# Performance work log

Hardware: AMD Instinct MI355X
Metric: run time of the kernel (lower is better)

The kernel has to match this reference:

```python
import jax, jax.numpy as jnp
import numpy as np

N, NFEAT, NHID, NCLASS, E = 100000, 128, 128, 40, 1600000

def _glorot(key, fan_in, fan_out):
    lim = float(np.sqrt(6.0 / (fan_in + fan_out)))
    return jax.random.uniform(key, (fan_in, fan_out), jnp.float32, -lim, lim)

def setup_inputs() -> dict:
    key = jax.random.key(0)
    ks = jax.random.split(key, 20)
    inp = {
        'x': jax.random.normal(ks[0], (N, NFEAT), jnp.float32),
        'edge_index': jax.random.randint(ks[1], (2, E), 0, N, jnp.int64 if jax.config.x64_enabled else jnp.int32),
    }
    dims = [(NFEAT, NHID), (NHID, NHID), (NHID, NHID), (NHID, NHID), (NHID, NHID), (NHID, NHID)]
    names = ['gc1_w1', 'gc1_w2', 'gc2_w1', 'gc2_w2', 'gc3_w1', 'gc3_w2']
    for i, (nm, (fi, fo)) in enumerate(zip(names, dims)):
        inp[nm] = _glorot(ks[2 + i], fi, fo)
        inp[nm.replace('w', 'b')] = jnp.zeros((fo,), jnp.float32)
    inp['lin1_w'] = _glorot(ks[10], 3 * NHID, 3 * NHID)
    inp['lin1_b'] = jnp.zeros((3 * NHID,), jnp.float32)
    inp['lin2_w'] = _glorot(ks[11], 3 * NHID, NCLASS)
    inp['lin2_b'] = jnp.zeros((NCLASS,), jnp.float32)
    return inp

def _gin_conv(x, src, dst, w1, b1, w2, b2):
    # GINConv, eps=0: mlp(x + sum_{j->i} x_j)
    agg = jax.ops.segment_sum(x[src], dst, num_segments=N)  # [N, d]
    h = jax.nn.relu((x + agg) @ w1 + b1)
    return jax.nn.relu(h @ w2 + b2)

def reference(x, edge_index, gc1_w1, gc1_b1, gc1_w2, gc1_b2,
              gc2_w1, gc2_b1, gc2_w2, gc2_b2,
              gc3_w1, gc3_b1, gc3_w2, gc3_b2,
              lin1_w, lin1_b, lin2_w, lin2_b):
    src, dst = edge_index[0], edge_index[1]
    h1 = _gin_conv(x, src, dst, gc1_w1, gc1_b1, gc1_w2, gc1_b2)
    h2 = _gin_conv(h1, src, dst, gc2_w1, gc2_b1, gc2_w2, gc2_b2)
    h3 = _gin_conv(h2, src, dst, gc3_w1, gc3_b1, gc3_w2, gc3_b2)
    h = jnp.concatenate([h1, h2, h3], axis=1)  # [N, 3*nhid]
    h = jax.nn.relu(h @ lin1_w + lin1_b)  # dropout inactive in eval mode
    h = h @ lin2_w + lin2_b
    return jax.nn.log_softmax(h, axis=1)
```

## Files before the change

kernel.cpp:

```cpp
#include <hip/hip_runtime.h>

#define N_NODES 100000
#define NEDGE   1600000
#define NHID    128
#define NCLASS  40

#define AGG_NODES 128
#define COLV_LDS  3072
#define FILL_RANGE  12500
#define WPREP_TOT   264192
#define EPB 2048
#define NBB 782
#define SUBN 782
#define NSUB 16

using bf16x8 = __attribute__((ext_vector_type(8))) short;
using f32x4  = __attribute__((ext_vector_type(4))) float;

__device__ __forceinline__ float bf2f(unsigned short s) {
    unsigned u = ((unsigned)s) << 16; float f; __builtin_memcpy(&f, &u, 4); return f;
}
__device__ __forceinline__ unsigned short f2bf(float f) {
    unsigned u; __builtin_memcpy(&u, &f, 4);
    u = u + 0x7fffu + ((u >> 16) & 1u);
    return (unsigned short)(u >> 16);
}

__device__ __forceinline__ void gld16(const void* g, void* l) {
    __builtin_amdgcn_global_load_lds(g, l, 16, 0, 0);
}

__global__ __launch_bounds__(256) void k_bucket(const int* __restrict__ ei,
                                                unsigned* __restrict__ pairs,
                                                int* __restrict__ bofs, int* __restrict__ bcnt) {
    __shared__ int wcnt[4][8];
    __shared__ int wbase[4][8];
    __shared__ int sbase[9];
    const int tid = threadIdx.x, lane = tid & 63, w = tid >> 6;
    const int e0 = blockIdx.x * EPB;
    const unsigned long long below = (1ull << lane) - 1ull;

    int dl[8], src[8], sl[8], posw[8];
    int cnt[8] = {0, 0, 0, 0, 0, 0, 0, 0};
    #pragma unroll
    for (int k = 0; k < 8; ++k) {
        int e = e0 + w * 512 + k * 64 + lane;
        bool v = e < NEDGE;
        int d = v ? ei[NEDGE + e] : -1;
        src[k] = v ? ei[e] : 0;
        int slc = v ? d / FILL_RANGE : -1;
        sl[k] = slc;
        dl[k] = v ? d - slc * FILL_RANGE : 0;
        posw[k] = 0;
        #pragma unroll
        for (int s = 0; s < 8; ++s) {
            unsigned long long mask = __ballot(slc == s);
            if (slc == s) posw[k] = cnt[s] + (int)__popcll(mask & below);
            cnt[s] += (int)__popcll(mask);
        }
    }
    if (lane == 0) {
        #pragma unroll
        for (int s = 0; s < 8; ++s) wcnt[w][s] = cnt[s];
    }
    __syncthreads();
    if (tid == 0) {
        int run = 0;
        for (int s = 0; s < 8; ++s) {
            sbase[s] = run;
            for (int w2 = 0; w2 < 4; ++w2) { wbase[w2][s] = run; run += wcnt[w2][s]; }
        }
        sbase[8] = run;
        for (int s = 0; s < 8; ++s) {
            bofs[blockIdx.x * 8 + s] = e0 + sbase[s];
            bcnt[blockIdx.x * 8 + s] = sbase[s + 1] - sbase[s];
        }
    }
    __syncthreads();
    #pragma unroll
    for (int k = 0; k < 8; ++k) {
        if (sl[k] >= 0)
            pairs[e0 + wbase[w][sl[k]] + posw[k]] = ((unsigned)dl[k] << 17) | (unsigned)src[k];
    }
}

__global__ void k_sseg(const int* __restrict__ bcnt, int* __restrict__ pbase, int* __restrict__ stot) {
    __shared__ int sh[256];
    const int s = blockIdx.x, t = threadIdx.x;
    int v[4]; int sum = 0;
    #pragma unroll
    for (int k = 0; k < 4; ++k) {
        int i = t * 4 + k;
        v[k] = (i < NBB) ? bcnt[i * 8 + s] : 0;
        sum += v[k];
    }
    sh[t] = sum; __syncthreads();
    for (int off = 1; off < 256; off <<= 1) {
        int x = (t >= off) ? sh[t - off] : 0;
        __syncthreads();
        sh[t] += x;
        __syncthreads();
    }
    int excl = sh[t] - sum;
    #pragma unroll
    for (int k = 0; k < 4; ++k) {
        int i = t * 4 + k;
        if (i < NBB) pbase[i * 8 + s] = excl;
        excl += v[k];
    }
    if (t == 255) stot[s] = sh[255];
}

__global__ void k_sbase(const int* __restrict__ stot, int* __restrict__ sbase,
                        unsigned* __restrict__ pairs2) {
    if (threadIdx.x || blockIdx.x) return;
    int run = 0;
    for (int s = 0; s < 8; ++s) {
        sbase[s] = run;
        int end = run + stot[s];
        run = (end + 3) & ~3;
        for (int i = end; i < run; ++i) pairs2[i] = 0xFFFFFFFFu;
    }
    sbase[8] = run;
}

__global__ __launch_bounds__(256) void k_scatter(const unsigned* __restrict__ pairs,
                                                 const int* __restrict__ bcnt,
                                                 const int* __restrict__ pbase,
                                                 const int* __restrict__ sbase,
                                                 unsigned* __restrict__ pairs2) {
    __shared__ int lb[9], ldst[8];
    const int bb = blockIdx.x, tid = threadIdx.x;
    if (tid == 0) {
        int run = 0;
        for (int s = 0; s < 8; ++s) {
            lb[s] = run; run += bcnt[bb * 8 + s];
            ldst[s] = sbase[s] + pbase[bb * 8 + s];
        }
        lb[8] = run;
    }
    __syncthreads();
    const int nblk = lb[8];
    for (int i = tid; i < nblk; i += 256) {
        int s = 0;
        #pragma unroll
        for (int j = 1; j < 8; ++j) s += (i >= lb[j]);
        pairs2[ldst[s] + (i - lb[s])] = pairs[(size_t)bb * EPB + i];
    }
}

__global__ __launch_bounds__(512) void k_cnt4(const unsigned* __restrict__ pairs2,
                                              const int* __restrict__ sbase,
                                              int* __restrict__ cnt) {
    __shared__ int lcnt[SUBN];
    const int s = blockIdx.x & 7, sub = blockIdx.x >> 3;
    const int nlo = sub * SUBN;
    const int nhi = (nlo + SUBN < FILL_RANGE) ? nlo + SUBN : FILL_RANGE;
    const int tid = threadIdx.x;
    for (int i = tid; i < SUBN; i += 512) lcnt[i] = 0;
    __syncthreads();
    const int beg = sbase[s];
    const int n4 = (sbase[s + 1] - beg) >> 2;
    const uint4* p4 = (const uint4*)(pairs2 + beg);
    for (int i = tid; i < n4; i += 512) {
        uint4 q = p4[i];
        int d0 = (int)(q.x >> 17), d1 = (int)(q.y >> 17);
        int d2 = (int)(q.z >> 17), d3 = (int)(q.w >> 17);
        if (d0 >= nlo && d0 < nhi) atomicAdd(&lcnt[d0 - nlo], 1);
        if (d1 >= nlo && d1 < nhi) atomicAdd(&lcnt[d1 - nlo], 1);
        if (d2 >= nlo && d2 < nhi) atomicAdd(&lcnt[d2 - nlo], 1);
        if (d3 >= nlo && d3 < nhi) atomicAdd(&lcnt[d3 - nlo], 1);
    }
    __syncthreads();
    const int base = s * FILL_RANGE + nlo;
    for (int i = tid; i < nhi - nlo; i += 512) cnt[base + i] = lcnt[i];
}

__global__ void k_scan1(const int* __restrict__ cnt, int* __restrict__ rp, int* __restrict__ bsum) {
    __shared__ int sh[256];
    int t = threadIdx.x, base = blockIdx.x * 1024;
    int v[4]; int s = 0;
    for (int k = 0; k < 4; ++k) { int i = base + t * 4 + k; v[k] = (i < N_NODES) ? cnt[i] : 0; s += v[k]; }
    sh[t] = s; __syncthreads();
    for (int off = 1; off < 256; off <<= 1) {
        int x = (t >= off) ? sh[t - off] : 0;
        __syncthreads();
        sh[t] += x;
        __syncthreads();
    }
    int excl = sh[t] - s;
    for (int k = 0; k < 4; ++k) { int i = base + t * 4 + k; if (i < N_NODES) rp[i] = excl; excl += v[k]; }
    if (t == 255) bsum[blockIdx.x] = sh[255];
}

__global__ void k_scan2(int* __restrict__ bsum, int nb) {
    __shared__ int sh[256];
    int t = threadIdx.x;
    int v = (t < nb) ? bsum[t] : 0;
    sh[t] = v; __syncthreads();
    for (int off = 1; off < 256; off <<= 1) {
        int x = (t >= off) ? sh[t - off] : 0;
        __syncthreads();
        sh[t] += x;
        __syncthreads();
    }
    if (t < nb) bsum[t] = sh[t] - v;
}

__global__ void k_scan3(int* __restrict__ rp, const int* __restrict__ bsum) {
    int base = blockIdx.x * 1024;
    int off = bsum[blockIdx.x];
    for (int k = 0; k < 4; ++k) {
        int i = base + threadIdx.x * 4 + k;
        if (i < N_NODES) rp[i] += off;
    }
    if (blockIdx.x == 0 && threadIdx.x == 0) rp[N_NODES] = NEDGE;
}

__global__ __launch_bounds__(512) void k_fill4(const unsigned* __restrict__ pairs2,
                                               const int* __restrict__ sbase,
                                               const int* __restrict__ rp,
                                               int* __restrict__ colv) {
    __shared__ int lcur[SUBN];
    __shared__ int lrp[SUBN];
    const int s = blockIdx.x & 7, sub = blockIdx.x >> 3;
    const int nlo = sub * SUBN;
    const int nhi = (nlo + SUBN < FILL_RANGE) ? nlo + SUBN : FILL_RANGE;
    const int tid = threadIdx.x;
    const int gbase = s * FILL_RANGE + nlo;
    for (int i = tid; i < SUBN; i += 512) {
        lcur[i] = 0;
        lrp[i] = (i < nhi - nlo) ? rp[gbase + i] : 0;
    }
    __syncthreads();
    const int beg = sbase[s];
    const int n4 = (sbase[s + 1] - beg) >> 2;
    const uint4* p4 = (const uint4*)(pairs2 + beg);
    for (int i = tid; i < n4; i += 512) {
        uint4 q = p4[i];
        unsigned e[4] = {q.x, q.y, q.z, q.w};
        #pragma unroll
        for (int k = 0; k < 4; ++k) {
            int dl = (int)(e[k] >> 17);
            if (dl >= nlo && dl < nhi) {
                int li = dl - nlo;
                int pos = atomicAdd(&lcur[li], 1);
                colv[lrp[li] + pos] = (int)(e[k] & 0x1FFFFu);
            }
        }
    }
}

__global__ void k_wprep_all(const float* __restrict__ g0, const float* __restrict__ g1,
                            const float* __restrict__ g2, const float* __restrict__ g3,
                            const float* __restrict__ g4, const float* __restrict__ g5,
                            const float* __restrict__ l1w, const float* __restrict__ l2w,
                            unsigned short* __restrict__ dst) {
    int idx = blockIdx.x * 256 + threadIdx.x;
    if (idx >= WPREP_TOT) return;
    const float* w; int local, K, O;
    if (idx < 98304) {
        int r = idx >> 14; local = idx & 16383; K = 128; O = 128;
        w = r == 0 ? g0 : r == 1 ? g1 : r == 2 ? g2 : r == 3 ? g3 : r == 4 ? g4 : g5;
    } else if (idx < 245760) {
        local = idx - 98304; K = 384; O = 384; w = l1w;
    } else {
        local = idx - 245760; K = 384; O = 40; w = l2w;
    }
    int kss = K >> 5;
    int e = local & 7, lane = (local >> 3) & 63, rest = local >> 9;
    int ks = rest % kss, ot = rest / kss;
    int c = ot * 16 + (lane & 15);
    int k = ks * 32 + (lane >> 4) * 8 + e;
    float v = (c < O) ? w[k * O + c] : 0.f;
    dst[idx] = f2bf(v);
}

__global__ void k_xprep(const float* __restrict__ x, unsigned short* __restrict__ xs) {
    int s = blockIdx.x & 3;
    int rest = (blockIdx.x >> 2) * 256 + threadIdx.x;
    if (rest >= N_NODES * 16) return;
    int n = rest >> 4, wrd = rest & 15;
    float2 v = *(const float2*)(x + (size_t)n * 128 + s * 32 + wrd * 2);
    ((unsigned*)xs)[(size_t)s * N_NODES * 16 + rest] =
        (unsigned)f2bf(v.x) | ((unsigned)f2bf(v.y) << 16);
}

__device__ __forceinline__ void acc8(float* acc, uint4 f, float m) {
    unsigned u[4] = {f.x, f.y, f.z, f.w};
    for (int d = 0; d < 4; ++d) {
        acc[2 * d]     = fmaf(m, bf2f((unsigned short)u[d]), acc[2 * d]);
        acc[2 * d + 1] = fmaf(m, bf2f((unsigned short)(u[d] >> 16)), acc[2 * d + 1]);
    }
}

__global__ __launch_bounds__(512) void k_aggs(const unsigned short* __restrict__ feat,
                                              unsigned short* __restrict__ tout,
                                              const int* __restrict__ rp,
                                              const int* __restrict__ colv) {
    __shared__ int scol[COLV_LDS + 8];
    __shared__ int srp[AGG_NODES + 1];
    const int s = blockIdx.x & 3;
    const int chunk = blockIdx.x >> 2;
    const int tid = threadIdx.x;
    const int nbase = chunk * AGG_NODES;

    for (int i = tid; i <= AGG_NODES; i += 512) {
        int n = nbase + i;
        srp[i] = rp[n <= N_NODES ? n : N_NODES];
    }
    __syncthreads();
    const int ebase = srp[0];
    const int ecount = srp[AGG_NODES] - ebase;
    const int elds = ecount < COLV_LDS ? ecount : COLV_LDS;
    for (int i = tid; i < elds; i += 512) scol[i] = colv[ebase + i];
    if (tid < 8) scol[elds + tid] = 0;
    __syncthreads();

    const unsigned* fs = (const unsigned*)feat + (size_t)s * N_NODES * 16;
    unsigned* ts = (unsigned*)tout + (size_t)s * N_NODES * 16;

    const int sub = tid >> 2, q = tid & 3;
    const int node = nbase + sub;
    if (node >= N_NODES) return;
    const int off = q * 4;
    const int e0 = srp[sub] - ebase, e1 = srp[sub + 1] - ebase;

    float acc[8];
    {
        uint4 a = *(const uint4*)(fs + (size_t)node * 16 + off);
        unsigned u[4] = {a.x, a.y, a.z, a.w};
        for (int d = 0; d < 4; ++d) {
            acc[2 * d]     = bf2f((unsigned short)u[d]);
            acc[2 * d + 1] = bf2f((unsigned short)(u[d] >> 16));
        }
    }

    if (ecount <= COLV_LDS) {
        int e = e0;
        const int efull = e0 + ((e1 - e0) & ~7);
        for (; e < efull; e += 8) {
            int j[8];
            #pragma unroll
            for (int k = 0; k < 8; ++k) j[k] = scol[e + k];
            uint4 f[8];
            #pragma unroll
            for (int k = 0; k < 8; ++k)
                f[k] = *(const uint4*)(fs + (size_t)j[k] * 16 + off);
            #pragma unroll
            for (int k = 0; k < 8; ++k) acc8(acc, f[k], 1.f);
        }
        if (e < e1) {
            int j[8]; float m[8];
            #pragma unroll
            for (int k = 0; k < 8; ++k) {
                int ee = e + k;
                bool v = ee < e1;
                j[k] = v ? scol[ee] : node;
                m[k] = v ? 1.f : 0.f;
            }
            uint4 f[8];
            #pragma unroll
            for (int k = 0; k < 8; ++k)
                f[k] = *(const uint4*)(fs + (size_t)j[k] * 16 + off);
            #pragma unroll
            for (int k = 0; k < 8; ++k) acc8(acc, f[k], m[k]);
        }
    } else {
        for (int e = e0; e < e1; e += 8) {
            int j[8]; float m[8];
            #pragma unroll
            for (int k = 0; k < 8; ++k) {
                int ee = e + k;
                bool v = ee < e1;
                int idx = ee < COLV_LDS ? scol[ee] : colv[ebase + ee];
                j[k] = v ? idx : node;
                m[k] = v ? 1.f : 0.f;
            }
            uint4 f[8];
            #pragma unroll
            for (int k = 0; k < 8; ++k)
                f[k] = *(const uint4*)(fs + (size_t)j[k] * 16 + off);
            #pragma unroll
            for (int k = 0; k < 8; ++k) acc8(acc, f[k], m[k]);
        }
    }

    uint4 o;
    o.x = (unsigned)f2bf(acc[0]) | ((unsigned)f2bf(acc[1]) << 16);
    o.y = (unsigned)f2bf(acc[2]) | ((unsigned)f2bf(acc[3]) << 16);
    o.z = (unsigned)f2bf(acc[4]) | ((unsigned)f2bf(acc[5]) << 16);
    o.w = (unsigned)f2bf(acc[6]) | ((unsigned)f2bf(acc[7]) << 16);
    *(uint4*)(ts + (size_t)node * 16 + off) = o;
}

__global__ __launch_bounds__(512) void k_mlp(
    const unsigned short* __restrict__ tin,
    const unsigned short* __restrict__ w1t, const float* __restrict__ b1,
    const unsigned short* __restrict__ w2t, const float* __restrict__ b2,
    unsigned short* __restrict__ hout) {
    __shared__ __align__(16) char tlds[4 * 8192];
    __shared__ __align__(16) char hlds[4 * 8192];
    const int tid = threadIdx.x, lane = tid & 63, w = tid >> 6;
    const int l15 = lane & 15, lg = lane >> 4;
    const int nbase = blockIdx.x * 128;
    const int rx = (l15 >> 1) & 3;

    #pragma unroll
    for (int i = 0; i < 4; ++i) {
        int c = w + i * 8;
        int s = c >> 3, rblk = c & 7;
        int node = nbase + rblk * 16 + (lane >> 2);
        if (node >= N_NODES) node = 0;
        int hsrc = (lane & 3) ^ ((lane >> 3) & 3);
        gld16(tin + ((size_t)s * N_NODES + node) * 32 + hsrc * 8,
              tlds + c * 1024);
    }

    bf16x8 B1[4], B2[4];
    const int col = w * 16 + l15;
    const float bias1 = b1[col], bias2 = b2[col];
    #pragma unroll
    for (int ks = 0; ks < 4; ++ks) {
        B1[ks] = *(const bf16x8*)(w1t + ((size_t)(w * 4 + ks) * 64 + lane) * 8);
        B2[ks] = *(const bf16x8*)(w2t + ((size_t)(w * 4 + ks) * 64 + lane) * 8);
    }
    __syncthreads();

    {
        const int hoff = ((lg ^ rx) << 4);
        bf16x8 A[2][4];
        #pragma unroll
        for (int ks = 0; ks < 4; ++ks)
            A[0][ks] = *(const bf16x8*)(tlds + ks * 8192 + l15 * 64 + hoff);
        #pragma unroll
        for (int m = 0; m < 8; ++m) {
            int cur = m & 1, nxt = cur ^ 1;
            if (m < 7) {
                int row = (m + 1) * 16 + l15;
                #pragma unroll
                for (int ks = 0; ks < 4; ++ks)
                    A[nxt][ks] = *(const bf16x8*)(tlds + ks * 8192 + row * 64 + hoff);
            }
            f32x4 acc = {0.f, 0.f, 0.f, 0.f};
            #pragma unroll
            for (int ks = 0; ks < 4; ++ks)
                acc = __builtin_amdgcn_mfma_f32_16x16x32_bf16(A[cur][ks], B1[ks], acc, 0, 0, 0);
            #pragma unroll
            for (int r = 0; r < 4; ++r) {
                int row = m * 16 + lg * 4 + r;
                int rw = (2 * lg + (r >> 1)) & 3;
                int h = (w & 1) * 2 + (l15 >> 3);
                float v = acc[r] + bias1; v = v > 0.f ? v : 0.f;
                *(unsigned short*)(hlds + (w >> 1) * 8192 + row * 64 +
                                   ((h ^ rw) << 4) + (l15 & 7) * 2) = f2bf(v);
            }
        }
    }
    __syncthreads();

    {
        const int hoff = ((lg ^ rx) << 4);
        bf16x8 A[2][4];
        #pragma unroll
        for (int ks = 0; ks < 4; ++ks)
            A[0][ks] = *(const bf16x8*)(hlds + ks * 8192 + l15 * 64 + hoff);
        #pragma unroll
        for (int m = 0; m < 8; ++m) {
            int cur = m & 1, nxt = cur ^ 1;
            if (m < 7) {
                int row = (m + 1) * 16 + l15;
                #pragma unroll
                for (int ks = 0; ks < 4; ++ks)
                    A[nxt][ks] = *(const bf16x8*)(hlds + ks * 8192 + row * 64 + hoff);
            }
            f32x4 acc = {0.f, 0.f, 0.f, 0.f};
            #pragma unroll
            for (int ks = 0; ks < 4; ++ks)
                acc = __builtin_amdgcn_mfma_f32_16x16x32_bf16(A[cur][ks], B2[ks], acc, 0, 0, 0);
            #pragma unroll
            for (int r = 0; r < 4; ++r) {
                int node = nbase + m * 16 + lg * 4 + r;
                if (node < N_NODES) {
                    float v = acc[r] + bias2; v = v > 0.f ? v : 0.f;
                    hout[((size_t)(w >> 1) * N_NODES + node) * 32 + (w & 1) * 16 + l15] = f2bf(v);
                }
            }
        }
    }
}

__global__ __launch_bounds__(512, 4) void k_final(
    const unsigned short* __restrict__ h1, const unsigned short* __restrict__ h2,
    const unsigned short* __restrict__ h3,
    const unsigned short* __restrict__ l1t, const float* __restrict__ l1b,
    const unsigned short* __restrict__ l2t, const float* __restrict__ l2b,
    float* __restrict__ out) {
    __shared__ __align__(16) char lds[12 * 4096];
    const int tid = threadIdx.x, lane = tid & 63, w = tid >> 6;
    const int l15 = lane & 15, lg = lane >> 4;
    const int nbase = blockIdx.x * 64;
    const int rx = (l15 >> 1) & 3;

    #pragma unroll
    for (int i = 0; i < 6; ++i) {
        int c = w + i * 8;
        int g = c >> 2, rblk = c & 3;
        int part = g >> 2, slice = g & 3;
        int node = nbase + rblk * 16 + (lane >> 2);
        if (node >= N_NODES) node = 0;
        int hsrc = (lane & 3) ^ ((lane >> 3) & 3);
        const unsigned short* hp = part == 0 ? h1 : (part == 1 ? h2 : h3);
        gld16(hp + ((size_t)slice * N_NODES + node) * 32 + hsrc * 8,
              lds + c * 1024);
    }

    bf16x8 B[2][3];
    #pragma unroll
    for (int ot = 0; ot < 3; ++ot)
        B[0][ot] = *(const bf16x8*)(l1t + ((size_t)((w * 3 + ot) * 12) * 64 + lane) * 8);
    __syncthreads();

    f32x4 acc[4][3];
    #pragma unroll
    for (int m = 0; m < 4; ++m)
        #pragma unroll
        for (int ot = 0; ot < 3; ++ot) acc[m][ot] = {0.f, 0.f, 0.f, 0.f};
    {
        const int hoff = ((lg ^ rx) << 4);
        #pragma unroll
        for (int ks = 0; ks < 12; ++ks) {
            int cur = ks & 1, nxt = cur ^ 1;
            if (ks < 11) {
                #pragma unroll
                for (int ot = 0; ot < 3; ++ot)
                    B[nxt][ot] = *(const bf16x8*)(l1t + ((size_t)((w * 3 + ot) * 12 + ks + 1) * 64 + lane) * 8);
            }
            bf16x8 A[4];
            #pragma unroll
            for (int m = 0; m < 4; ++m) {
                int row = m * 16 + l15;
                A[m] = *(const bf16x8*)(lds + ks * 4096 + row * 64 + hoff);
            }
            #pragma unroll
            for (int ot = 0; ot < 3; ++ot)
                #pragma unroll
                for (int m = 0; m < 4; ++m)
                    acc[m][ot] = __builtin_amdgcn_mfma_f32_16x16x32_bf16(A[m], B[cur][ot], acc[m][ot], 0, 0, 0);
        }
    }
    __syncthreads();

    #pragma unroll
    for (int ot = 0; ot < 3; ++ot) {
        int c = (w * 3 + ot) * 16 + l15;
        int gc = c >> 5, h = (c >> 3) & 3, b2i = (c & 7) * 2;
        float bias = l1b[c];
        #pragma unroll
        for (int m = 0; m < 4; ++m)
            #pragma unroll
            for (int r = 0; r < 4; ++r) {
                int row = m * 16 + lg * 4 + r;
                int rw = (2 * lg + (r >> 1)) & 3;
                float v = acc[m][ot][r] + bias; v = v > 0.f ? v : 0.f;
                *(unsigned short*)(lds + gc * 4096 + row * 64 + ((h ^ rw) << 4) + b2i) = f2bf(v);
            }
    }
    __syncthreads();

    if (w < 4) {
        f32x4 acc2[3];
        #pragma unroll
        for (int ot = 0; ot < 3; ++ot) acc2[ot] = {0.f, 0.f, 0.f, 0.f};
        {
            const int row = w * 16 + l15;
            const int hoff = ((lg ^ rx) << 4);
            bf16x8 C2[2][3];
            #pragma unroll
            for (int ot = 0; ot < 3; ++ot)
                C2[0][ot] = *(const bf16x8*)(l2t + ((size_t)(ot * 12) * 64 + lane) * 8);
            #pragma unroll
            for (int ks = 0; ks < 12; ++ks) {
                int cur = ks & 1, nxt = cur ^ 1;
                if (ks < 11) {
                    #pragma unroll
                    for (int ot = 0; ot < 3; ++ot)
                        C2[nxt][ot] = *(const bf16x8*)(l2t + ((size_t)(ot * 12 + ks + 1) * 64 + lane) * 8);
                }
                bf16x8 A2 = *(const bf16x8*)(lds + ks * 4096 + row * 64 + hoff);
                #pragma unroll
                for (int ot = 0; ot < 3; ++ot)
                    acc2[ot] = __builtin_amdgcn_mfma_f32_16x16x32_bf16(A2, C2[cur][ot], acc2[ot], 0, 0, 0);
            }
        }

        int c0 = l15;
        #pragma unroll
        for (int r = 0; r < 4; ++r) {
            float v0 = acc2[0][r] + l2b[c0];
            float v1 = acc2[1][r] + l2b[c0 + 16];
            float v2 = (c0 < 8) ? (acc2[2][r] + l2b[c0 + 32]) : -1e30f;
            float mx = fmaxf(fmaxf(v0, v1), v2);
            for (int msk = 1; msk < 16; msk <<= 1) mx = fmaxf(mx, __shfl_xor(mx, msk));
            float s = __expf(v0 - mx) + __expf(v1 - mx) + ((c0 < 8) ? __expf(v2 - mx) : 0.f);
            for (int msk = 1; msk < 16; msk <<= 1) s += __shfl_xor(s, msk);
            float lse = mx + __logf(s);
            int node = nbase + w * 16 + lg * 4 + r;
            if (node < N_NODES) {
                out[(size_t)node * 40 + c0] = v0 - lse;
                out[(size_t)node * 40 + c0 + 16] = v1 - lse;
                if (c0 < 8) out[(size_t)node * 40 + c0 + 32] = v2 - lse;
            }
        }
    }
}

extern "C" void kernel_launch(void* const* d_in, const int* in_sizes, int n_in,
                              void* d_out, int out_size, void* d_ws, size_t ws_size,
                              hipStream_t stream) {
    const float* x  = (const float*)d_in[0];
    const int*   ei = (const int*)d_in[1];
    const float* gw1[3] = {(const float*)d_in[2],  (const float*)d_in[6],  (const float*)d_in[10]};
    const float* gb1[3] = {(const float*)d_in[3],  (const float*)d_in[7],  (const float*)d_in[11]};
    const float* gw2[3] = {(const float*)d_in[4],  (const float*)d_in[8],  (const float*)d_in[12]};
    const float* gb2[3] = {(const float*)d_in[5],  (const float*)d_in[9],  (const float*)d_in[13]};
    const float* l1w = (const float*)d_in[14];
    const float* l1b = (const float*)d_in[15];
    const float* l2w = (const float*)d_in[16];
    const float* l2b = (const float*)d_in[17];
    float* out = (float*)d_out;

    char* p = (char*)d_ws;
    auto alloc = [&](size_t bytes) { char* q = p; p += (bytes + 255) & ~(size_t)255; return q; };
    int* rp    = (int*)alloc(4 * (N_NODES + 1));
    int* cnt   = (int*)alloc(4 * N_NODES);
    int* bsum  = (int*)alloc(4 * 256);
    int* bofs  = (int*)alloc(4 * NBB * 8);
    int* bcnt  = (int*)alloc(4 * NBB * 8);
    int* pbase = (int*)alloc(4 * NBB * 8);
    int* stot  = (int*)alloc(4 * 16);
    int* sbase = (int*)alloc(4 * 16);
    unsigned* pairs  = (unsigned*)alloc(4 * (size_t)NEDGE);
    unsigned* pairs2 = (unsigned*)alloc(4 * ((size_t)NEDGE + 64));
    int* colv  = (int*)alloc(4 * (size_t)NEDGE);
    unsigned short* t  = (unsigned short*)alloc(2 * (size_t)N_NODES * 128);
    unsigned short* h1 = (unsigned short*)alloc(2 * (size_t)N_NODES * 128);
    unsigned short* h2 = (unsigned short*)alloc(2 * (size_t)N_NODES * 128);
    unsigned short* h3 = (unsigned short*)alloc(2 * (size_t)N_NODES * 128);
    unsigned short* xs = h3;
    unsigned short* wt[6];
    for (int i = 0; i < 6; ++i) wt[i] = (unsigned short*)alloc(2 * 128 * 128);
    unsigned short* l1t = (unsigned short*)alloc(2 * 384 * 384);
    unsigned short* l2t = (unsigned short*)alloc(2 * 48 * 384);

    const int nb = (N_NODES + 1023) / 1024;
    k_bucket<<<NBB, 256, 0, stream>>>(ei, pairs, bofs, bcnt);
    k_sseg<<<8, 256, 0, stream>>>(bcnt, pbase, stot);
    k_sbase<<<1, 64, 0, stream>>>(stot, sbase, pairs2);
    k_scatter<<<NBB, 256, 0, stream>>>(pairs, bcnt, pbase, sbase, pairs2);
    k_cnt4<<<8 * NSUB, 512, 0, stream>>>(pairs2, sbase, cnt);
    k_scan1<<<nb, 256, 0, stream>>>(cnt, rp, bsum);
    k_scan2<<<1, 256, 0, stream>>>(bsum, nb);
    k_scan3<<<nb, 256, 0, stream>>>(rp, bsum);
    k_fill4<<<8 * NSUB, 512, 0, stream>>>(pairs2, sbase, rp, colv);

    k_wprep_all<<<(WPREP_TOT + 255) / 256, 256, 0, stream>>>(
        gw1[0], gw2[0], gw1[1], gw2[1], gw1[2], gw2[2], l1w, l2w, wt[0]);

    k_xprep<<<4 * ((N_NODES * 16 + 255) / 256), 256, 0, stream>>>(x, xs);

    const int gagg = ((N_NODES + AGG_NODES - 1) / AGG_NODES) * 4;
    const int gtile2 = (N_NODES + 127) / 128;
    const int gtile1 = (N_NODES + 63) / 64;
    k_aggs<<<gagg, 512, 0, stream>>>(xs, t, rp, colv);
    k_mlp<<<gtile2, 512, 0, stream>>>(t, wt[0], gb1[0], wt[1], gb2[0], h1);
    k_aggs<<<gagg, 512, 0, stream>>>(h1, t, rp, colv);
    k_mlp<<<gtile2, 512, 0, stream>>>(t, wt[2], gb1[1], wt[3], gb2[1], h2);
    k_aggs<<<gagg, 512, 0, stream>>>(h2, t, rp, colv);
    k_mlp<<<gtile2, 512, 0, stream>>>(t, wt[4], gb1[2], wt[5], gb2[2], h3);
    k_final<<<gtile1, 512, 0, stream>>>(h1, h2, h3, l1t, l1b, l2t, l2b, out);
}
```

Measured before the change: 443.9 us.

## Balance aggregation by splitting block edges evenly across thread groups with LDS atomics

After: 689.9 us. +55.4%, slower.

```diff
diff --git a/kernel.cpp b/kernel.cpp
--- a/kernel.cpp
+++ b/kernel.cpp
@@ -300,6 +300,7 @@
                                               const int* __restrict__ colv) {
     __shared__ int scol[COLV_LDS + 8];
     __shared__ int srp[AGG_NODES + 1];
+    __shared__ float facc[AGG_NODES * 32];
     const int s = blockIdx.x & 3;
     const int chunk = blockIdx.x >> 2;
     const int tid = threadIdx.x;
@@ -309,6 +310,7 @@
         int n = nbase + i;
         srp[i] = rp[n <= N_NODES ? n : N_NODES];
     }
+    for (int i = tid; i < AGG_NODES * 32; i += 512) facc[i] = 0.f;
     __syncthreads();
     const int ebase = srp[0];
     const int ecount = srp[AGG_NODES] - ebase;
@@ -320,78 +322,86 @@
     const unsigned* fs = (const unsigned*)feat + (size_t)s * N_NODES * 16;
     unsigned* ts = (unsigned*)tout + (size_t)s * N_NODES * 16;
 
-    const int sub = tid >> 2, q = tid & 3;
-    const int node = nbase + sub;
-    if (node >= N_NODES) return;
+    const int g = tid >> 2, q = tid & 3;
     const int off = q * 4;
-    const int e0 = srp[sub] - ebase, e1 = srp[sub + 1] - ebase;
-
-    float acc[8];
-    {
-        uint4 a = *(const uint4*)(fs + (size_t)node * 16 + off);
-        unsigned u[4] = {a.x, a.y, a.z, a.w};
-        for (int d = 0; d < 4; ++d) {
-            acc[2 * d]     = bf2f((unsigned short)u[d]);
-            acc[2 * d + 1] = bf2f((unsigned short)(u[d] >> 16));
-        }
-    }
-
-    if (ecount <= COLV_LDS) {
-        int e = e0;
-        const int efull = e0 + ((e1 - e0) & ~7);
-        for (; e < efull; e += 8) {
+    const int fcol = q * 8;
+    const int stripe = (ecount + AGG_NODES - 1) >> 7;
+    int gbeg = ebase + g * stripe;
+    int gend = ebase + ecount;
+    if (gbeg + stripe < gend) gend = gbeg + stripe;
+
+    if (gbeg < gend) {
+        int lo = 0, hi = AGG_NODES;
+        while (hi - lo > 1) {
+            int mid = (lo + hi) >> 1;
+            if (srp[mid] <= gbeg) lo = mid; else hi = mid;
+        }
+        int node = lo;
+        float acc[8];
+        #pragma unroll
+        for (int d = 0; d < 8; ++d) acc[d] = 0.f;
+        bool any = false;
+        for (int e = gbeg; e < gend; e += 8) {
             int j[8];
             #pragma unroll
-            for (int k = 0; k < 8; ++k) j[k] = scol[e + k];
+            for (int k = 0; k < 8; ++k) {
+                int eg = e + k;
+                int li = eg - ebase;
+                int lic = (eg < gend) ? li : 0;
+                j[k] = (lic < COLV_LDS) ? scol[lic] : colv[ebase + lic];
+            }
             uint4 f[8];
             #pragma unroll
             for (int k = 0; k < 8; ++k)
                 f[k] = *(const uint4*)(fs + (size_t)j[k] * 16 + off);
             #pragma unroll
-            for (int k = 0; k < 8; ++k) acc8(acc, f[k], 1.f);
-        }
-        if (e < e1) {
-            int j[8]; float m[8];
-            #pragma unroll
             for (int k = 0; k < 8; ++k) {
-                int ee = e + k;
-                bool v = ee < e1;
-                j[k] = v ? scol[ee] : node;
-                m[k] = v ? 1.f : 0.f;
-            }
-            uint4 f[8];
-            #pragma unroll
-            for (int k = 0; k < 8; ++k)
-                f[k] = *(const uint4*)(fs + (size_t)j[k] * 16 + off);
-            #pragma unroll
-            for (int k = 0; k < 8; ++k) acc8(acc, f[k], m[k]);
-        }
-    } else {
-        for (int e = e0; e < e1; e += 8) {
-            int j[8]; float m[8];
-            #pragma unroll
-            for (int k = 0; k < 8; ++k) {
-                int ee = e + k;
-                bool v = ee < e1;
-                int idx = ee < COLV_LDS ? scol[ee] : colv[ebase + ee];
-                j[k] = v ? idx : node;
-                m[k] = v ? 1.f : 0.f;
-            }
-            uint4 f[8];
-            #pragma unroll
-            for (int k = 0; k < 8; ++k)
-                f[k] = *(const uint4*)(fs + (size_t)j[k] * 16 + off);
-            #pragma unroll
-            for (int k = 0; k < 8; ++k) acc8(acc, f[k], m[k]);
-        }
-    }
-
-    uint4 o;
-    o.x = (unsigned)f2bf(acc[0]) | ((unsigned)f2bf(acc[1]) << 16);
-    o.y = (unsigned)f2bf(acc[2]) | ((unsigned)f2bf(acc[3]) << 16);
-    o.z = (unsigned)f2bf(acc[4]) | ((unsigned)f2bf(acc[5]) << 16);
-    o.w = (unsigned)f2bf(acc[6]) | ((unsigned)f2bf(acc[7]) << 16);
-    *(uint4*)(ts + (size_t)node * 16 + off) = o;
+                int eg = e + k;
+                if (eg < gend) {
+                    while (eg >= srp[node + 1]) {
+                        if (any) {
+                            #pragma unroll
+                            for (int d = 0; d < 8; ++d)
+                                atomicAdd(&facc[node * 32 + fcol + d], acc[d]);
+                            #pragma unroll
+                            for (int d = 0; d < 8; ++d) acc[d] = 0.f;
+                            any = false;
+                        }
+                        ++node;
+                    }
+                    acc8(acc, f[k], 1.f);
+                    any = true;
+                }
+            }
+        }
+        if (any) {
+            #pragma unroll
+            for (int d = 0; d < 8; ++d)
+                atomicAdd(&facc[node * 32 + fcol + d], acc[d]);
+        }
+    }
+    __syncthreads();
+
+    {
+        int node = tid >> 2;
+        int ng = nbase + node;
+        if (ng < N_NODES) {
+            uint4 a = *(const uint4*)(fs + (size_t)ng * 16 + off);
+            unsigned u[4] = {a.x, a.y, a.z, a.w};
+            float o[8];
+            #pragma unroll
+            for (int d = 0; d < 4; ++d) {
+                o[2 * d]     = bf2f((unsigned short)u[d])         + facc[node * 32 + fcol + 2 * d];
+                o[2 * d + 1] = bf2f((unsigned short)(u[d] >> 16)) + facc[node * 32 + fcol + 2 * d + 1];
+            }
+            uint4 wv;
+            wv.x = (unsigned)f2bf(o[0]) | ((unsigned)f2bf(o[1]) << 16);
+            wv.y = (unsigned)f2bf(o[2]) | ((unsigned)f2bf(o[3]) << 16);
+            wv.z = (unsigned)f2bf(o[4]) | ((unsigned)f2bf(o[5]) << 16);
+            wv.w = (unsigned)f2bf(o[6]) | ((unsigned)f2bf(o[7]) << 16);
+            *(uint4*)(ts + (size_t)ng * 16 + off) = wv;
+        }
+    }
 }
 
 __global__ __launch_bounds__(512) void k_mlp(
```
